# Optimization experiments

Measured on AMD Instinct MI355X. Metric: run time of the kernel, lower is better.

Reference implementation:

```python
import jax, jax.numpy as jnp
import numpy as np

B, C, H, W = 4, 1024, 64, 64
N_ROIS = 256
STRIDE = 16


def setup_inputs() -> dict:
    key = jax.random.key(0)
    k1, k2, kx1, kx2, ky1, ky2 = jax.random.split(key, 6)
    std_base_feat = jax.random.normal(k1, (B, C, H, W), dtype=jnp.float32)
    tch_base_feat = jax.random.normal(k2, (B, C, H, W), dtype=jnp.float32)
    # ROIs in image coordinates: (batch_idx, x1, y1, x2, y2), coords in [0, W*stride)
    xa = jax.random.randint(kx1, (B, N_ROIS), 0, W * STRIDE).astype(jnp.float32)
    xb = jax.random.randint(kx2, (B, N_ROIS), 0, W * STRIDE).astype(jnp.float32)
    ya = jax.random.randint(ky1, (B, N_ROIS), 0, H * STRIDE).astype(jnp.float32)
    yb = jax.random.randint(ky2, (B, N_ROIS), 0, H * STRIDE).astype(jnp.float32)
    bidx = jnp.broadcast_to(jnp.arange(B, dtype=jnp.float32)[:, None], (B, N_ROIS))
    rois = jnp.stack(
        [bidx,
         jnp.minimum(xa, xb), jnp.minimum(ya, yb),
         jnp.maximum(xa, xb), jnp.maximum(ya, yb)], axis=-1)  # [B, N, 5]
    return {"std_base_feat": std_base_feat, "tch_base_feat": tch_base_feat,
            "rois": rois, "stride": STRIDE}


def reference(std_base_feat, tch_base_feat, rois, stride):
    b, c, h, w = std_base_feat.shape
    n = rois.shape[1]
    # int() truncation in the original; coords are non-negative so floor == trunc
    x1 = jnp.floor(rois[..., 1] / stride).astype(jnp.int32)  # [B, N]
    y1 = jnp.floor(rois[..., 2] / stride).astype(jnp.int32)
    x2 = jnp.floor(rois[..., 3] / stride).astype(jnp.int32)
    y2 = jnp.floor(rois[..., 4] / stride).astype(jnp.int32)
    valid = (y2 > y1) & (x2 > x1)  # [B, N]

    # per-pixel channel-summed squared diff: [B, H, W]
    diff2 = jnp.sum((std_base_feat - tch_base_feat) ** 2, axis=1)

    ys = jnp.arange(h)  # [H]
    xs = jnp.arange(w)  # [W]
    mask_y = (ys[None, None, :] >= y1[..., None]) & (ys[None, None, :] <= y2[..., None])  # [B,N,H]
    mask_x = (xs[None, None, :] >= x1[..., None]) & (xs[None, None, :] <= x2[..., None])  # [B,N,W]
    mask = (mask_y[..., :, None] & mask_x[..., None, :]).astype(diff2.dtype)  # [B,N,H,W]

    roi_sse = jnp.einsum('bnhw,bhw->bn', mask, diff2)  # sum of sq diff per crop
    area = ((y2 - y1 + 1) * (x2 - x1 + 1)).astype(diff2.dtype)
    roi_mse = roi_sse / (c * area)  # MSELoss (mean) per crop

    mse_loss = jnp.sum(jnp.where(valid, roi_mse, 0.0)) / (b * n)
    return mse_loss
```

## Files before the change

### kernel.cpp

```cpp
#include <hip/hip_runtime.h>

constexpr int Bv = 4;
constexpr int Cv = 1024;
constexpr int Hv = 64;
constexpr int Wv = 64;
constexpr int NROIS = 256;
constexpr int HWv = Hv * Wv;
constexpr int PIX = Bv * HWv;
constexpr int G = 16;
constexpr int CPG = Cv / G;

__global__ __launch_bounds__(256) void k_diff2_partial(
    const float* __restrict__ std_f, const float* __restrict__ tch_f,
    float* __restrict__ partial) {
  int t = blockIdx.x * blockDim.x + threadIdx.x;
  int g = t >> 12;
  int v = t & 4095;
  int p = v << 2;
  int b = p >> 12;
  int hw = p & 4095;

  const float* ps = std_f + ((size_t)b * Cv + (size_t)g * CPG) * HWv + hw;
  const float* pt = tch_f + ((size_t)b * Cv + (size_t)g * CPG) * HWv + hw;

  float4 acc = make_float4(0.f, 0.f, 0.f, 0.f);
#pragma unroll 4
  for (int c = 0; c < CPG; ++c) {
    float4 s = *reinterpret_cast<const float4*>(ps + (size_t)c * HWv);
    float4 q = *reinterpret_cast<const float4*>(pt + (size_t)c * HWv);
    float dx = s.x - q.x, dy = s.y - q.y, dz = s.z - q.z, dw = s.w - q.w;
    acc.x += dx * dx;
    acc.y += dy * dy;
    acc.z += dz * dz;
    acc.w += dw * dw;
  }
  *reinterpret_cast<float4*>(partial + (size_t)g * PIX + p) = acc;
}

__global__ __launch_bounds__(256) void k_diff2_reduce(
    const float* __restrict__ partial, float* __restrict__ diff2) {
  int p = blockIdx.x * blockDim.x + threadIdx.x;
  float acc = 0.f;
#pragma unroll
  for (int g = 0; g < G; ++g) acc += partial[(size_t)g * PIX + p];
  diff2[p] = acc;
}

__device__ __forceinline__ float block_reduce_256(float v) {
  for (int off = 32; off > 0; off >>= 1) v += __shfl_down(v, off, 64);
  __shared__ float smem[4];
  int lane = threadIdx.x & 63;
  int wid = threadIdx.x >> 6;
  if (lane == 0) smem[wid] = v;
  __syncthreads();
  float r = 0.f;
  if (threadIdx.x == 0) r = smem[0] + smem[1] + smem[2] + smem[3];
  return r;
}

__global__ __launch_bounds__(256) void k_roi_mse(
    const float* __restrict__ diff2, const float* __restrict__ rois,
    const int* __restrict__ stride_p, float* __restrict__ roi_out) {
  int roi_id = blockIdx.x;
  int b = roi_id >> 8;
  const float* r = rois + (size_t)roi_id * 5;
  float inv_stride = 1.0f / (float)stride_p[0];

  int x1 = (int)floorf(r[1] * inv_stride);
  int y1 = (int)floorf(r[2] * inv_stride);
  int x2 = (int)floorf(r[3] * inv_stride);
  int y2 = (int)floorf(r[4] * inv_stride);

  bool valid = (y2 > y1) && (x2 > x1);
  if (!valid) {
    if (threadIdx.x == 0) roi_out[roi_id] = 0.f;
    return;
  }

  int wroi = x2 - x1 + 1;
  int hroi = y2 - y1 + 1;
  int area = wroi * hroi;

  const float* d2 = diff2 + (size_t)b * HWv;
  float acc = 0.f;
  for (int idx = threadIdx.x; idx < area; idx += 256) {
    int yy = y1 + idx / wroi;
    int xx = x1 + idx % wroi;
    acc += d2[yy * Wv + xx];
  }
  float sse = block_reduce_256(acc);
  if (threadIdx.x == 0) {
    roi_out[roi_id] = sse / ((float)Cv * (float)area);
  }
}

__global__ __launch_bounds__(256) void k_final(
    const float* __restrict__ roi_out, float* __restrict__ out) {
  float acc = 0.f;
#pragma unroll
  for (int i = 0; i < (Bv * NROIS) / 256; ++i)
    acc += roi_out[i * 256 + threadIdx.x];
  float total = block_reduce_256(acc);
  if (threadIdx.x == 0) out[0] = total / (float)(Bv * NROIS);
}

extern "C" void kernel_launch(void* const* d_in, const int* in_sizes, int n_in,
                              void* d_out, int out_size, void* d_ws,
                              size_t ws_size, hipStream_t stream) {
  const float* std_f = (const float*)d_in[0];
  const float* tch_f = (const float*)d_in[1];
  const float* rois = (const float*)d_in[2];
  const int* stride_p = (const int*)d_in[3];
  float* out = (float*)d_out;

  float* partial = (float*)d_ws;
  float* diff2 = partial + (size_t)G * PIX;
  float* roi_out = diff2 + PIX;

  k_diff2_partial<<<(G * PIX / 4) / 256, 256, 0, stream>>>(std_f, tch_f,
                                                           partial);
  k_diff2_reduce<<<PIX / 256, 256, 0, stream>>>(partial, diff2);
  k_roi_mse<<<Bv * NROIS, 256, 0, stream>>>(diff2, rois, stride_p, roi_out);
  k_final<<<1, 256, 0, stream>>>(roi_out, out);
}
```

Measured before the change: 32.40 us.

## Fold partial-sum reduction into ROI kernel and finalize with atomics

Removes the separate channel-group reduce kernel and the final single-block reduction, so only two kernels launch. Each ROI block now sums directly over all channel-group partial planes, and the per-ROI mean is accumulated into the output with an atomic add after the first kernel zeroes it. The channel-group count is doubled and unrolling increased in the streaming kernel. This cuts launch overhead and intermediate writes, at the cost of much redundant partial reads per ROI and nondeterministic float summation order.

```diff
diff --git a/kernel.cpp b/kernel.cpp
--- a/kernel.cpp
+++ b/kernel.cpp
@@ -7,13 +7,15 @@
 constexpr int NROIS = 256;
 constexpr int HWv = Hv * Wv;
 constexpr int PIX = Bv * HWv;
-constexpr int G = 16;
+constexpr int G = 32;
 constexpr int CPG = Cv / G;
 
 __global__ __launch_bounds__(256) void k_diff2_partial(
     const float* __restrict__ std_f, const float* __restrict__ tch_f,
-    float* __restrict__ partial) {
-  int t = blockIdx.x * blockDim.x + threadIdx.x;
+    float* __restrict__ partial, float* __restrict__ out) {
+  if (blockIdx.x == 0 && threadIdx.x == 0) out[0] = 0.f;
+
+  int t = blockIdx.x * 256 + threadIdx.x;
   int g = t >> 12;
   int v = t & 4095;
   int p = v << 2;
@@ -24,7 +26,7 @@
   const float* pt = tch_f + ((size_t)b * Cv + (size_t)g * CPG) * HWv + hw;
 
   float4 acc = make_float4(0.f, 0.f, 0.f, 0.f);
-#pragma unroll 4
+#pragma unroll 8
   for (int c = 0; c < CPG; ++c) {
     float4 s = *reinterpret_cast<const float4*>(ps + (size_t)c * HWv);
     float4 q = *reinterpret_cast<const float4*>(pt + (size_t)c * HWv);
@@ -35,15 +37,6 @@
     acc.w += dw * dw;
   }
   *reinterpret_cast<float4*>(partial + (size_t)g * PIX + p) = acc;
-}
-
-__global__ __launch_bounds__(256) void k_diff2_reduce(
-    const float* __restrict__ partial, float* __restrict__ diff2) {
-  int p = blockIdx.x * blockDim.x + threadIdx.x;
-  float acc = 0.f;
-#pragma unroll
-  for (int g = 0; g < G; ++g) acc += partial[(size_t)g * PIX + p];
-  diff2[p] = acc;
 }
 
 __device__ __forceinline__ float block_reduce_256(float v) {
@@ -59,8 +52,8 @@
 }
 
 __global__ __launch_bounds__(256) void k_roi_mse(
-    const float* __restrict__ diff2, const float* __restrict__ rois,
-    const int* __restrict__ stride_p, float* __restrict__ roi_out) {
+    const float* __restrict__ partial, const float* __restrict__ rois,
+    const int* __restrict__ stride_p, float* __restrict__ out) {
   int roi_id = blockIdx.x;
   int b = roi_id >> 8;
   const float* r = rois + (size_t)roi_id * 5;
@@ -71,37 +64,28 @@
   int x2 = (int)floorf(r[3] * inv_stride);
   int y2 = (int)floorf(r[4] * inv_stride);
 
-  bool valid = (y2 > y1) && (x2 > x1);
-  if (!valid) {
-    if (threadIdx.x == 0) roi_out[roi_id] = 0.f;
-    return;
-  }
+  if (!((y2 > y1) && (x2 > x1))) return;
 
   int wroi = x2 - x1 + 1;
   int hroi = y2 - y1 + 1;
   int area = wroi * hroi;
 
-  const float* d2 = diff2 + (size_t)b * HWv;
   float acc = 0.f;
-  for (int idx = threadIdx.x; idx < area; idx += 256) {
-    int yy = y1 + idx / wroi;
-    int xx = x1 + idx % wroi;
-    acc += d2[yy * Wv + xx];
+  const float* base = partial + (size_t)b * HWv;
+#pragma unroll
+  for (int g = 0; g < G; ++g) {
+    const float* pg = base + (size_t)g * PIX;
+    for (int idx = threadIdx.x; idx < area; idx += 256) {
+      int yy = y1 + idx / wroi;
+      int xx = x1 + idx % wroi;
+      acc += pg[yy * Wv + xx];
+    }
   }
   float sse = block_reduce_256(acc);
   if (threadIdx.x == 0) {
-    roi_out[roi_id] = sse / ((float)Cv * (float)area);
+    float mse = sse / ((float)Cv * (float)area);
+    atomicAdd(out, mse / (float)(Bv * NROIS));
   }
-}
-
-__global__ __launch_bounds__(256) void k_final(
-    const float* __restrict__ roi_out, float* __restrict__ out) {
-  float acc = 0.f;
-#pragma unroll
-  for (int i = 0; i < (Bv * NROIS) / 256; ++i)
-    acc += roi_out[i * 256 + threadIdx.x];
-  float total = block_reduce_256(acc);
-  if (threadIdx.x == 0) out[0] = total / (float)(Bv * NROIS);
 }
 
 extern "C" void kernel_launch(void* const* d_in, const int* in_sizes, int n_in,
@@ -114,12 +98,8 @@
   float* out = (float*)d_out;
 
   float* partial = (float*)d_ws;
-  float* diff2 = partial + (size_t)G * PIX;
-  float* roi_out = diff2 + PIX;
 
-  k_diff2_partial<<<(G * PIX / 4) / 256, 256, 0, stream>>>(std_f, tch_f,
-                                                           partial);
-  k_diff2_reduce<<<PIX / 256, 256, 0, stream>>>(partial, diff2);
-  k_roi_mse<<<Bv * NROIS, 256, 0, stream>>>(diff2, rois, stride_p, roi_out);
-  k_final<<<1, 256, 0, stream>>>(roi_out, out);
+  k_diff2_partial<<<G * (PIX / 4) / 256, 256, 0, stream>>>(std_f, tch_f,
+                                                           partial, out);
+  k_roi_mse<<<Bv * NROIS, 256, 0, stream>>>(partial, rois, stride_p, out);
 }
```

New measurement: 95.98 us. 196% more time.
